# Kernel optimization log

Hardware: AMD Instinct MI355X
Metric: run time of the kernel (lower is better)

## Reference

```python
import jax, jax.numpy as jnp
import numpy as np

DIM = 128          # channel dim of lst/gui
MASK_INDIM = 64    # FCNet input dim
H = 512
W = 512
SE_RED = 16        # SELayer reduction


def setup_inputs() -> dict:
    key = jax.random.key(0)
    ks = jax.random.split(key, 16)
    s = 0.05
    d, md = DIM, MASK_INDIM
    half = d // 2
    se_hid = (2 * d) // SE_RED
    return {
        "lst": jax.random.normal(ks[0], (1, d, H, W), jnp.float32),
        "gui": jax.random.normal(ks[1], (1, d, H, W), jnp.float32),
        "mask": jax.random.normal(ks[2], (1, md), jnp.float32),
        # FCNet(mask_indim, dim, num_filts=dim): Linear -> ReLU -> Linear
        "w1": jax.random.normal(ks[3], (md, d), jnp.float32) * s,
        "b1": jnp.zeros((d,), jnp.float32),
        "w2": jax.random.normal(ks[4], (d, d), jnp.float32) * s,
        "b2": jnp.zeros((d,), jnp.float32),
        # SELayer(2*dim, reduction=16): pool -> Linear(2d, 2d/16) -> ReLU -> Linear(., d) -> sigmoid
        "se_w1": jax.random.normal(ks[5], (2 * d, se_hid), jnp.float32) * s,
        "se_b1": jnp.zeros((se_hid,), jnp.float32),
        "se_w2": jax.random.normal(ks[6], (se_hid, d), jnp.float32) * s,
        "se_b2": jnp.zeros((d,), jnp.float32),
        # 1x1 convs on dim//2 channels -> plain [out, in] matrices
        "conv1_w": jax.random.normal(ks[7], (half, half), jnp.float32) * s,
        "conv1_b": jnp.zeros((half,), jnp.float32),
        "conv2_w": jax.random.normal(ks[8], (half, half), jnp.float32) * s,
        "conv2_b": jnp.zeros((half,), jnp.float32),
    }


def reference(lst, gui, mask, w1, b1, w2, b2, se_w1, se_b1, se_w2, se_b2,
              conv1_w, conv1_b, conv2_w, conv2_b):
    # mask1: FCNet + sigmoid -> [1, C]
    mask1 = jax.nn.sigmoid(jnp.maximum(mask @ w1 + b1, 0.0) @ w2 + b2)
    # mask2: SE on cat([lst, gui], dim=1) -> global avg pool -> MLP -> [1, C]
    pooled = jnp.concatenate([lst.mean((2, 3)), gui.mean((2, 3))], axis=1)  # [1, 2C]
    mask2 = jax.nn.sigmoid(jnp.maximum(pooled @ se_w1 + se_b1, 0.0) @ se_w2 + se_b2)
    m = mask1 * mask2  # [1, C]

    C = m.shape[1]
    k = C // 2
    _, idx = jax.lax.top_k(m[0], k)
    idx = jnp.sort(idx)  # boolean gather in torch returns channels in ascending index order

    # 1x1 convs applied to the k selected channels (treated as an unbatched image)
    o_lst = jnp.einsum('oi,ihw->ohw', conv2_w, gui[0, idx]) + conv2_b[:, None, None]
    o_gui = jnp.einsum('oi,ihw->ohw', conv1_w, lst[0, idx]) + conv1_b[:, None, None]

    # scatter exchanged channels back; unselected channels pass through
    out_lst = lst.at[0, idx].set(o_lst)
    out_gui = gui.at[0, idx].set(o_gui)
    return out_lst, out_gui, m
```

## Files before the change

kernel.cpp:

```cpp
#include <hip/hip_runtime.h>

#define NPIX (512*512)
#define N4   (NPIX/4)
#define DIM  128
#define HALF 64
#define CHW  ((size_t)DIM*NPIX)

__global__ __launch_bounds__(1024) void k_means(const float* __restrict__ lst,
                                                const float* __restrict__ gui,
                                                float* __restrict__ means) {
    int b = blockIdx.x;
    const float* src = (b < DIM) ? (lst + (size_t)b * NPIX)
                                 : (gui + (size_t)(b - DIM) * NPIX);
    const float4* s4 = (const float4*)src;
    int t = threadIdx.x;
    float sum = 0.f;
#pragma unroll 8
    for (int k = 0; k < 64; ++k) {
        float4 v = s4[t + k * 1024];
        sum += (v.x + v.y) + (v.z + v.w);
    }
    for (int off = 32; off > 0; off >>= 1)
        sum += __shfl_down(sum, off, 64);
    __shared__ float red[16];
    int wave = t >> 6, lane = t & 63;
    if (lane == 0) red[wave] = sum;
    __syncthreads();
    if (t == 0) {
        float tot = 0.f;
        for (int w = 0; w < 16; ++w) tot += red[w];
        means[b] = tot * (1.0f / (float)NPIX);
    }
}

__global__ __launch_bounds__(128) void k_select(
    const float* __restrict__ mask, const float* __restrict__ w1, const float* __restrict__ b1,
    const float* __restrict__ w2, const float* __restrict__ b2,
    const float* __restrict__ se_w1, const float* __restrict__ se_b1,
    const float* __restrict__ se_w2, const float* __restrict__ se_b2,
    const float* __restrict__ means,
    float* __restrict__ m_out, int* __restrict__ idx_out, int* __restrict__ pos_out)
{
    int t = threadIdx.x;
    __shared__ float smask[64], h[128], pooled[256], se1[16], mv[128];
    __shared__ int sel[128];

    if (t < 64) smask[t] = mask[t];
    pooled[t]       = means[t];
    pooled[t + 128] = means[t + 128];
    __syncthreads();

    float a = b1[t];
    for (int i = 0; i < 64; ++i) a = fmaf(smask[i], w1[i * DIM + t], a);
    h[t] = fmaxf(a, 0.f);
    __syncthreads();

    float a2 = b2[t];
    for (int i = 0; i < 128; ++i) a2 = fmaf(h[i], w2[i * DIM + t], a2);
    float m1 = 1.f / (1.f + expf(-a2));

    if (t < 16) {
        float b = se_b1[t];
        for (int i = 0; i < 256; ++i) b = fmaf(pooled[i], se_w1[i * 16 + t], b);
        se1[t] = fmaxf(b, 0.f);
    }
    __syncthreads();

    float a3 = se_b2[t];
    for (int i = 0; i < 16; ++i) a3 = fmaf(se1[i], se_w2[i * DIM + t], a3);
    float m2 = 1.f / (1.f + expf(-a3));

    float mval = m1 * m2;
    mv[t] = mval;
    m_out[t] = mval;
    __syncthreads();

    int rank = 0;
    for (int i = 0; i < 128; ++i) {
        float o = mv[i];
        rank += (o > mval) || (o == mval && i < t);
    }
    int is_sel = (rank < HALF) ? 1 : 0;
    sel[t] = is_sel;
    __syncthreads();
    int pos = 0;
    for (int i = 0; i < t; ++i) pos += sel[i];
    pos_out[t] = is_sel ? pos : -1;
    if (is_sel) idx_out[pos] = t;
}

__device__ __forceinline__ void fma4(float4& a, float s, const float4& x) {
    a.x = fmaf(s, x.x, a.x);
    a.y = fmaf(s, x.y, a.y);
    a.z = fmaf(s, x.z, a.z);
    a.w = fmaf(s, x.w, a.w);
}

__global__ __launch_bounds__(256) void k_exchange(
    const float* __restrict__ lst, const float* __restrict__ gui,
    const float* __restrict__ c1w, const float* __restrict__ c1b,
    const float* __restrict__ c2w, const float* __restrict__ c2b,
    const int* __restrict__ idx,
    float* __restrict__ out)
{
    int z = blockIdx.y;
    const float* w    = (z == 0) ? c2w : c1w;
    const float* bias = (z == 0) ? c2b : c1b;
    const float4* src4 = (const float4*)((z == 0) ? gui : lst);
    float4* dst4 = (float4*)(out + (size_t)z * CHW);

    __shared__ float wT[HALF * HALF];
    __shared__ float bs[HALF];
    __shared__ int idxs[HALF];
    int tid = threadIdx.x;
    for (int k = tid; k < HALF * HALF; k += 256) {
        int o = k >> 6, i = k & 63;
        wT[i * HALF + o] = w[k];
    }
    if (tid < HALF) { bs[tid] = bias[tid]; idxs[tid] = idx[tid]; }
    __syncthreads();

    int tx = tid & 63;
    int ty = tid >> 6;
    int jbase = ty * 16;
    int p4 = blockIdx.x * 64 + tx;

    const float4* wT4 = (const float4*)wT;

    float4 acc[16];
#pragma unroll
    for (int j = 0; j < 16; ++j) {
        float b = bs[jbase + j];
        acc[j] = make_float4(b, b, b, b);
    }

#pragma unroll 2
    for (int i = 0; i < HALF; ++i) {
        int c = idxs[i];
        float4 x = src4[(size_t)c * N4 + p4];
#pragma unroll
        for (int q = 0; q < 4; ++q) {
            float4 w4 = wT4[i * 16 + ty * 4 + q];
            fma4(acc[q * 4 + 0], w4.x, x);
            fma4(acc[q * 4 + 1], w4.y, x);
            fma4(acc[q * 4 + 2], w4.z, x);
            fma4(acc[q * 4 + 3], w4.w, x);
        }
    }

#pragma unroll
    for (int j = 0; j < 16; ++j) {
        int c = idxs[jbase + j];
        dst4[(size_t)c * N4 + p4] = acc[j];
    }
}

__global__ __launch_bounds__(256) void k_copy(
    const float* __restrict__ lst, const float* __restrict__ gui,
    const int* __restrict__ pos, float* __restrict__ out)
{
    int c = blockIdx.y;
    int z = blockIdx.z;
    if (pos[c] >= 0) return;
    const float4* src4 = (const float4*)(((z == 0) ? lst : gui) + (size_t)c * NPIX);
    float4* dst4 = (float4*)(out + (size_t)z * CHW + (size_t)c * NPIX);
    int p4 = blockIdx.x * 256 + threadIdx.x;
    dst4[p4] = src4[p4];
}

extern "C" void kernel_launch(void* const* d_in, const int* in_sizes, int n_in,
                              void* d_out, int out_size, void* d_ws, size_t ws_size,
                              hipStream_t stream) {
    const float* lst   = (const float*)d_in[0];
    const float* gui   = (const float*)d_in[1];
    const float* mask  = (const float*)d_in[2];
    const float* w1    = (const float*)d_in[3];
    const float* b1    = (const float*)d_in[4];
    const float* w2    = (const float*)d_in[5];
    const float* b2    = (const float*)d_in[6];
    const float* se_w1 = (const float*)d_in[7];
    const float* se_b1 = (const float*)d_in[8];
    const float* se_w2 = (const float*)d_in[9];
    const float* se_b2 = (const float*)d_in[10];
    const float* c1w   = (const float*)d_in[11];
    const float* c1b   = (const float*)d_in[12];
    const float* c2w   = (const float*)d_in[13];
    const float* c2b   = (const float*)d_in[14];
    float* out = (float*)d_out;

    float* means = (float*)d_ws;
    int* idx     = (int*)((char*)d_ws + 1024);
    int* pos     = (int*)((char*)d_ws + 1024 + 256);

    k_means<<<dim3(256), dim3(1024), 0, stream>>>(lst, gui, means);
    k_select<<<dim3(1), dim3(128), 0, stream>>>(mask, w1, b1, w2, b2,
                                                se_w1, se_b1, se_w2, se_b2,
                                                means, out + 2 * CHW, idx, pos);
    k_exchange<<<dim3(NPIX / 256, 2), dim3(256), 0, stream>>>(lst, gui, c1w, c1b, c2w, c2b,
                                                              idx, out);
    k_copy<<<dim3(N4 / 256, 128, 2), dim3(256), 0, stream>>>(lst, gui, pos, out);
}
```

Baseline: 578.6 us.

## Fuse passthrough copy into exchange kernel and use nontemporal stores

Drops the separate copy kernel. The exchange kernel now also copies the unselected channels for its pixel tile, using an unselected-channel index list that the select kernel writes out. Output stores become nontemporal so they do not pollute the cache. This removes one launch and the copy grid's early-exit blocks, but adds per-thread register and memory pressure to the exchange kernel.

```diff
diff --git a/kernel.cpp b/kernel.cpp
--- a/kernel.cpp
+++ b/kernel.cpp
@@ -5,6 +5,13 @@
 #define DIM  128
 #define HALF 64
 #define CHW  ((size_t)DIM*NPIX)
+
+typedef float v4f __attribute__((ext_vector_type(4)));
+
+__device__ __forceinline__ void nt_store4(const float4& v, float4* p) {
+    v4f x; x.x = v.x; x.y = v.y; x.z = v.z; x.w = v.w;
+    __builtin_nontemporal_store(x, (v4f*)p);
+}
 
 __global__ __launch_bounds__(1024) void k_means(const float* __restrict__ lst,
                                                 const float* __restrict__ gui,
@@ -39,7 +46,7 @@
     const float* __restrict__ se_w1, const float* __restrict__ se_b1,
     const float* __restrict__ se_w2, const float* __restrict__ se_b2,
     const float* __restrict__ means,
-    float* __restrict__ m_out, int* __restrict__ idx_out, int* __restrict__ pos_out)
+    float* __restrict__ m_out, int* __restrict__ idx_out, int* __restrict__ uidx_out)
 {
     int t = threadIdx.x;
     __shared__ float smask[64], h[128], pooled[256], se1[16], mv[128];
@@ -85,8 +92,8 @@
     __syncthreads();
     int pos = 0;
     for (int i = 0; i < t; ++i) pos += sel[i];
-    pos_out[t] = is_sel ? pos : -1;
     if (is_sel) idx_out[pos] = t;
+    else        uidx_out[t - pos] = t;
 }
 
 __device__ __forceinline__ void fma4(float4& a, float s, const float4& x) {
@@ -96,28 +103,30 @@
     a.w = fmaf(s, x.w, a.w);
 }
 
-__global__ __launch_bounds__(256) void k_exchange(
+__global__ __launch_bounds__(256) void k_fused(
     const float* __restrict__ lst, const float* __restrict__ gui,
     const float* __restrict__ c1w, const float* __restrict__ c1b,
     const float* __restrict__ c2w, const float* __restrict__ c2b,
-    const int* __restrict__ idx,
+    const int* __restrict__ idx, const int* __restrict__ uidx,
     float* __restrict__ out)
 {
     int z = blockIdx.y;
     const float* w    = (z == 0) ? c2w : c1w;
     const float* bias = (z == 0) ? c2b : c1b;
-    const float4* src4 = (const float4*)((z == 0) ? gui : lst);
+    const float4* conv_src = (const float4*)((z == 0) ? gui : lst);
+    const float4* copy_src = (const float4*)((z == 0) ? lst : gui);
     float4* dst4 = (float4*)(out + (size_t)z * CHW);
 
     __shared__ float wT[HALF * HALF];
     __shared__ float bs[HALF];
     __shared__ int idxs[HALF];
+    __shared__ int uidxs[HALF];
     int tid = threadIdx.x;
     for (int k = tid; k < HALF * HALF; k += 256) {
         int o = k >> 6, i = k & 63;
         wT[i * HALF + o] = w[k];
     }
-    if (tid < HALF) { bs[tid] = bias[tid]; idxs[tid] = idx[tid]; }
+    if (tid < HALF) { bs[tid] = bias[tid]; idxs[tid] = idx[tid]; uidxs[tid] = uidx[tid]; }
     __syncthreads();
 
     int tx = tid & 63;
@@ -137,7 +146,7 @@
 #pragma unroll 2
     for (int i = 0; i < HALF; ++i) {
         int c = idxs[i];
-        float4 x = src4[(size_t)c * N4 + p4];
+        float4 x = conv_src[(size_t)c * N4 + p4];
 #pragma unroll
         for (int q = 0; q < 4; ++q) {
             float4 w4 = wT4[i * 16 + ty * 4 + q];
@@ -151,21 +160,19 @@
 #pragma unroll
     for (int j = 0; j < 16; ++j) {
         int c = idxs[jbase + j];
-        dst4[(size_t)c * N4 + p4] = acc[j];
-    }
-}
-
-__global__ __launch_bounds__(256) void k_copy(
-    const float* __restrict__ lst, const float* __restrict__ gui,
-    const int* __restrict__ pos, float* __restrict__ out)
-{
-    int c = blockIdx.y;
-    int z = blockIdx.z;
-    if (pos[c] >= 0) return;
-    const float4* src4 = (const float4*)(((z == 0) ? lst : gui) + (size_t)c * NPIX);
-    float4* dst4 = (float4*)(out + (size_t)z * CHW + (size_t)c * NPIX);
-    int p4 = blockIdx.x * 256 + threadIdx.x;
-    dst4[p4] = src4[p4];
+        nt_store4(acc[j], &dst4[(size_t)c * N4 + p4]);
+    }
+
+#pragma unroll
+    for (int r = 0; r < 2; ++r) {
+        float4 v[8];
+#pragma unroll
+        for (int j = 0; j < 8; ++j)
+            v[j] = copy_src[(size_t)uidxs[jbase + r * 8 + j] * N4 + p4];
+#pragma unroll
+        for (int j = 0; j < 8; ++j)
+            nt_store4(v[j], &dst4[(size_t)uidxs[jbase + r * 8 + j] * N4 + p4]);
+    }
 }
 
 extern "C" void kernel_launch(void* const* d_in, const int* in_sizes, int n_in,
@@ -190,13 +197,12 @@
 
     float* means = (float*)d_ws;
     int* idx     = (int*)((char*)d_ws + 1024);
-    int* pos     = (int*)((char*)d_ws + 1024 + 256);
+    int* uidx    = (int*)((char*)d_ws + 1024 + 256);
 
     k_means<<<dim3(256), dim3(1024), 0, stream>>>(lst, gui, means);
     k_select<<<dim3(1), dim3(128), 0, stream>>>(mask, w1, b1, w2, b2,
                                                 se_w1, se_b1, se_w2, se_b2,
-                                                means, out + 2 * CHW, idx, pos);
-    k_exchange<<<dim3(NPIX / 256, 2), dim3(256), 0, stream>>>(lst, gui, c1w, c1b, c2w, c2b,
-                                                              idx, out);
-    k_copy<<<dim3(N4 / 256, 128, 2), dim3(256), 0, stream>>>(lst, gui, pos, out);
-}
+                                                means, out + 2 * CHW, idx, uidx);
+    k_fused<<<dim3(NPIX / 256, 2), dim3(256), 0, stream>>>(lst, gui, c1w, c1b, c2w, c2b,
+                                                           idx, uidx, out);
+}
```

After: 537.3 us. -7.1%, faster.
